# Kernel tuning notes

Measured on AMD Instinct MI355X. Metric: run time of the kernel, lower is better.

Reference implementation:

```python
import jax, jax.numpy as jnp
import numpy as np

T, D, I, E, G, LG, K = 2048, 1024, 512, 32, 8, 4, 6
SI = 2 * I  # shared expert inter dim = n_shared_experts * inter_dim
ROUTE_SCALE = 1.0


def setup_inputs() -> dict:
    key = jax.random.key(0)
    ks = jax.random.split(key, 16)
    s = 0.02
    f = jnp.float32
    return {
        "x": jax.random.normal(ks[0], (T, D), f),
        "router_w": jax.random.normal(ks[1], (E, D), f) * s,
        "router_b": jax.random.normal(ks[2], (E,), f) * s,
        "W1": jax.random.normal(ks[3], (E, D, I), f) * s,
        "b1": jax.random.normal(ks[4], (E, I), f) * s,
        "W2": jax.random.normal(ks[5], (E, D, I), f) * s,
        "b2": jax.random.normal(ks[6], (E, I), f) * s,
        "W3": jax.random.normal(ks[7], (E, I, D), f) * s,
        "b3": jax.random.normal(ks[8], (E, D), f) * s,
        "sw1": jax.random.normal(ks[9], (D, SI), f) * s,
        "sb1": jax.random.normal(ks[10], (SI,), f) * s,
        "sw2": jax.random.normal(ks[11], (D, SI), f) * s,
        "sb2": jax.random.normal(ks[12], (SI,), f) * s,
        "sw3": jax.random.normal(ks[13], (SI, D), f) * s,
        "sb3": jax.random.normal(ks[14], (D,), f) * s,
    }


def _route(x, router_w, router_b):
    # Router: softmax scores (fp32), group-limited top-k.
    logits = x @ router_w.T + router_b                      # [T, E]
    scores = jax.nn.softmax(logits.astype(jnp.float32), axis=-1)
    original = scores
    sg = scores.reshape(x.shape[0], G, E // G)              # [T, G, E/G]
    # no router bias -> group score = sum of top-2 expert scores per group
    group_scores = jnp.sum(jax.lax.top_k(sg, 2)[0], axis=-1)  # [T, G]
    _, gidx = jax.lax.top_k(group_scores, LG)               # [T, LG]
    keep = jnp.zeros((x.shape[0], G), bool).at[jnp.arange(x.shape[0])[:, None], gidx].set(True)
    masked = jnp.where(keep[:, :, None], sg, -jnp.inf).reshape(x.shape[0], E)
    _, idx = jax.lax.top_k(masked, K)                       # [T, K]
    vals = jnp.take_along_axis(original, idx, axis=1) * ROUTE_SCALE
    return vals.astype(x.dtype), idx


def reference(x, router_w, router_b, W1, b1, W2, b2, W3, b3, sw1, sb1, sw2, sb2, sw3, sb3):
    vals, idx = _route(x, router_w, router_b)
    # dense gate matrix [T, E]; top-k indices per row are distinct
    gates = jnp.zeros((x.shape[0], E), x.dtype).at[jnp.arange(x.shape[0])[:, None], idx].set(vals)
    # routed experts: Expert(x) = W3 @ silu(w1(x) * w2(x))
    h1 = jnp.einsum('td,edi->tei', x, W1) + b1              # [T, E, I]
    h2 = jnp.einsum('td,edi->tei', x, W2) + b2
    h = jax.nn.silu(h1 * h2)
    y = jnp.einsum('tei,eid->td', h * gates[:, :, None], W3) + gates @ b3
    # shared expert
    z = jax.nn.silu((x @ sw1 + sb1) * (x @ sw2 + sb2)) @ sw3 + sb3
    return y + z
```

## Files before the change

### kernel.cpp

```cpp
#include <hip/hip_runtime.h>
#include <hip/hip_bf16.h>
#include <math.h>

#define T_CONST 2048
#define D_CONST 1024
#define I_CONST 512
#define SI_CONST 1024
#define E_CONST 32
#define G_CONST 8
#define LG_CONST 4
#define KSEL 6
#define BK 32

typedef __attribute__((ext_vector_type(8))) short short8;
typedef __attribute__((ext_vector_type(4))) float floatx4;

__device__ inline unsigned pack_bf16(float a, float b) {
  __hip_bfloat162 h = __float22bfloat162_rn(float2{a, b});
  return *reinterpret_cast<unsigned*>(&h);
}

__device__ inline void gload16(const void* g, void* l) {
  __builtin_amdgcn_global_load_lds(
      (const __attribute__((address_space(1))) unsigned int*)g,
      (__attribute__((address_space(3))) unsigned int*)l, 16, 0, 0);
}

__global__ __launch_bounds__(256) void cvt_x(const float* __restrict__ in,
                                             __hip_bfloat16* __restrict__ out) {
  size_t i = ((size_t)blockIdx.x * 256 + threadIdx.x) * 4;
  float4 v = *(const float4*)&in[i];
  uint2 u{pack_bf16(v.x, v.y), pack_bf16(v.z, v.w)};
  *(uint2*)&out[i] = u;
}

__global__ __launch_bounds__(256) void cvt_rwt(const float* __restrict__ rw,
                                               float* __restrict__ rwt) {
  int i = blockIdx.x * 256 + threadIdx.x;
  int d = i >> 5, e = i & 31;
  rwt[d * 32 + e] = rw[e * D_CONST + d];
}

__global__ __launch_bounds__(256) void transpose_all(
    const float* __restrict__ W1, const float* __restrict__ W2,
    const float* __restrict__ W3, const float* __restrict__ sw1,
    const float* __restrict__ sw2, const float* __restrict__ sw3,
    __hip_bfloat16* __restrict__ W1t, __hip_bfloat16* __restrict__ W2t,
    __hip_bfloat16* __restrict__ W3t, __hip_bfloat16* __restrict__ sw1t,
    __hip_bfloat16* __restrict__ sw2t, __hip_bfloat16* __restrict__ sw3t) {
  __shared__ short tile[64 * 64];
  int b = blockIdx.x;
  const float* in;
  __hip_bfloat16* out;
  int K, N, k0, n0;
  if (b < 8192) {
    int local = b & 4095;
    int mat = local >> 7, rem = local & 127;
    K = 1024; N = 512;
    in = ((b < 4096) ? W1 : W2) + (size_t)mat * (1024 * 512);
    out = ((b < 4096) ? W1t : W2t) + (size_t)mat * (1024 * 512);
    n0 = (rem & 7) * 64; k0 = (rem >> 3) * 64;
  } else if (b < 12288) {
    int local = b - 8192;
    int mat = local >> 7, rem = local & 127;
    K = 512; N = 1024;
    in = W3 + (size_t)mat * (512 * 1024);
    out = W3t + (size_t)mat * (512 * 1024);
    n0 = (rem & 15) * 64; k0 = (rem >> 4) * 64;
  } else {
    int local = b - 12288;
    int which = local >> 8, rem = local & 255;
    K = 1024; N = 1024;
    in = which == 0 ? sw1 : which == 1 ? sw2 : sw3;
    out = which == 0 ? sw1t : which == 1 ? sw2t : sw3t;
    n0 = (rem & 15) * 64; k0 = (rem >> 4) * 64;
  }
  const int tid = threadIdx.x;
  const int u = tid & 15, tr = tid >> 4;
  float4 v[4];
#pragma unroll
  for (int r = 0; r < 4; ++r)
    v[r] = *(const float4*)&in[(size_t)(k0 + 4 * tr + r) * N + n0 + 4 * u];
#pragma unroll
  for (int j = 0; j < 4; ++j) {
    int n = 4 * u + j;
    unsigned lo = pack_bf16(((const float*)&v[0])[j], ((const float*)&v[1])[j]);
    unsigned hi = pack_bf16(((const float*)&v[2])[j], ((const float*)&v[3])[j]);
    int cu = (tr >> 1) ^ (u & 7);
    int off = n * 64 + cu * 8 + (tr & 1) * 4;
    *(uint2*)&tile[off] = uint2{lo, hi};
  }
  __syncthreads();
#pragma unroll
  for (int s2 = 0; s2 < 2; ++s2) {
    int id = tid + s2 * 256;
    int n = id >> 3, cu = id & 7;
    int cx = cu ^ ((n >> 2) & 7);
    uint4 o = *(const uint4*)&tile[n * 64 + cx * 8];
    *(uint4*)&out[(size_t)(n0 + n) * K + k0 + cu * 8] = o;
  }
}

__global__ __launch_bounds__(256) void router2(
    const float* __restrict__ x, const float* __restrict__ rwt,
    const float* __restrict__ rb, int* __restrict__ counts,
    int* __restrict__ stok, float* __restrict__ gatel) {
  const int lane = threadIdx.x & 63;
  const int wv = threadIdx.x >> 6;
  const int t = blockIdx.x * 4 + wv;
  const int e = lane & 31, h = lane >> 5;
  const float* xp = x + (size_t)t * D_CONST;
  float s = 0.f;
#pragma unroll 8
  for (int d = h; d < D_CONST; d += 2) s = fmaf(xp[d], rwt[d * 32 + e], s);
  s += __shfl_xor(s, 32);
  s += rb[e];
  float mx = s;
#pragma unroll
  for (int m = 16; m >= 1; m >>= 1) mx = fmaxf(mx, __shfl_xor(mx, m));
  float p = expf(s - mx);
  float sum = p;
#pragma unroll
  for (int m = 16; m >= 1; m >>= 1) sum += __shfl_xor(sum, m);
  float sc = p / sum;
  float a = sc, bb = __shfl_xor(a, 1);
  float hi = fmaxf(a, bb), lo = fminf(a, bb);
  float oh = __shfl_xor(hi, 2), ol = __shfl_xor(lo, 2);
  float gs = fmaxf(fmaxf(hi + oh, hi + lo), oh + ol);
  const int g = e >> 2;
  unsigned keep = 0;
  float gv = gs;
#pragma unroll
  for (int r = 0; r < LG_CONST; ++r) {
    float v = gv;
    int gi = g;
#pragma unroll
    for (int m = 16; m >= 1; m >>= 1) {
      float ov = __shfl_xor(v, m);
      int og = __shfl_xor(gi, m);
      if (ov > v || (ov == v && og < gi)) { v = ov; gi = og; }
    }
    keep |= 1u << gi;
    if (g == gi) gv = -1e30f;
  }
  float cand = ((keep >> g) & 1u) ? sc : -1e30f;
  int sel_e = -1;
  float sel_v = 0.f;
#pragma unroll
  for (int r = 0; r < KSEL; ++r) {
    float v = cand;
    int ei = e;
#pragma unroll
    for (int m = 16; m >= 1; m >>= 1) {
      float ov = __shfl_xor(v, m);
      int oe = __shfl_xor(ei, m);
      if (ov > v || (ov == v && oe < ei)) { v = ov; ei = oe; }
    }
    if (lane == r) { sel_e = ei; sel_v = v; }
    if (e == ei) cand = -1e30f;
  }
  if (lane < KSEL) {
    int pos = atomicAdd(&counts[sel_e], 1);
    stok[sel_e * T_CONST + pos] = t;
    gatel[sel_e * T_CONST + pos] = sel_v;
  }
}

__global__ __launch_bounds__(64) void plan_build(
    const int* __restrict__ counts, int* __restrict__ offsets,
    int* __restrict__ plan_up, int* __restrict__ plan_dn, int* __restrict__ meta) {
  const int lane = threadIdx.x;
  for (int i = lane; i < 128; i += 64) {
    int ent = (E_CONST << 8) | i;
    plan_up[i] = ent;
    plan_dn[i] = ent;
  }
  int cnt = (lane < E_CONST) ? counts[lane] : 0;
  int incl = cnt;
#pragma unroll
  for (int d = 1; d < 64; d <<= 1) {
    int v = __shfl_up(incl, d);
    if (lane >= d) incl += v;
  }
  if (lane < E_CONST) offsets[lane] = incl - cnt;
  if (lane == E_CONST - 1) offsets[E_CONST] = incl;
  int mbs = (cnt + 127) >> 7;
  int pm = mbs;
#pragma unroll
  for (int d = 1; d < 64; d <<= 1) {
    int v = __shfl_up(pm, d);
    if (lane >= d) pm += v;
  }
  int pmex = pm - mbs;
  if (lane < E_CONST) {
    int ub = 128 + pmex * 4, db = 128 + pmex * 8;
    for (int mb = 0; mb < mbs; ++mb) {
#pragma unroll
      for (int nb = 0; nb < 4; ++nb)
        plan_up[ub + mb * 4 + nb] = (lane << 8) | (mb << 3) | nb;
#pragma unroll
      for (int nb = 0; nb < 8; ++nb)
        plan_dn[db + mb * 8 + nb] = (lane << 8) | (mb << 3) | nb;
    }
  }
  if (lane == E_CONST - 1) {
    meta[0] = 128 + pm * 4;
    meta[1] = 128 + pm * 8;
  }
}

__global__ __launch_bounds__(256) void gather_x(
    const __hip_bfloat16* __restrict__ xbf, const int* __restrict__ counts,
    const int* __restrict__ offsets, const int* __restrict__ stok,
    const float* __restrict__ gatel, __hip_bfloat16* __restrict__ Xg,
    float* __restrict__ cgate, int* __restrict__ tcnt, int* __restrict__ tslot) {
  int e = blockIdx.x;
  int cnt = counts[e];
  int row = blockIdx.y * 16 + (threadIdx.x >> 4);
  if (row >= cnt) return;
  int seg = threadIdx.x & 15;
  int tok = stok[e * T_CONST + row];
  int dst = offsets[e] + row;
  const uint4* src = (const uint4*)(xbf + (size_t)tok * D_CONST);
  uint4* d = (uint4*)(Xg + (size_t)dst * D_CONST);
#pragma unroll
  for (int i = 0; i < 8; ++i) d[i * 16 + seg] = src[i * 16 + seg];
  if (seg == 0) {
    cgate[dst] = gatel[e * T_CONST + row];
    int sl = atomicAdd(&tcnt[tok], 1);
    tslot[tok * 8 + sl] = dst;
  }
}

__global__ __launch_bounds__(256, 2) void up_fused(
    const __hip_bfloat16* __restrict__ Xg, const __hip_bfloat16* __restrict__ xbf,
    const __hip_bfloat16* __restrict__ W1t, const __hip_bfloat16* __restrict__ W2t,
    const __hip_bfloat16* __restrict__ sw1t, const __hip_bfloat16* __restrict__ sw2t,
    const float* __restrict__ b1, const float* __restrict__ b2,
    const float* __restrict__ sb1, const float* __restrict__ sb2,
    const int* __restrict__ counts, const int* __restrict__ offsets,
    const int* __restrict__ plan, const int* __restrict__ meta,
    __hip_bfloat16* __restrict__ He, __hip_bfloat16* __restrict__ Hs) {
  const int nw = meta[0];
  const int bx = blockIdx.x;
  if (bx >= nw) return;
  const int q = nw >> 3, r = nw & 7, c = bx & 7, sl = bx >> 3;
  const int j = (c < r ? c * (q + 1) : r * (q + 1) + (c - r) * q) + sl;
  const int ent = plan[j];
  const int z = ent >> 8;
  const int m0 = ((ent >> 3) & 31) * 128;
  const int n0 = (ent & 7) * 128;
  const bool SH = (z == E_CONST);
  const int cnt = SH ? T_CONST : counts[z];
  const int base = SH ? 0 : offsets[z];

  const __hip_bfloat16* Ab = SH ? (xbf + (size_t)m0 * D_CONST)
                                : (Xg + (size_t)(base + m0) * D_CONST);
  const __hip_bfloat16* B1 = SH ? (sw1t + (size_t)n0 * D_CONST)
                                : (W1t + ((size_t)z * I_CONST + n0) * D_CONST);
  const __hip_bfloat16* B2 = SH ? (sw2t + (size_t)n0 * D_CONST)
                                : (W2t + ((size_t)z * I_CONST + n0) * D_CONST);

  __shared__ short As[3 * 4096], Bs1[3 * 4096], Bs2[3 * 4096];

  const int tid = threadIdx.x, lane = tid & 63, wv = tid >> 6;
  const int l15 = lane & 15, quad = lane >> 4;
  const int wm = wv & 1, wn = wv >> 1;
  const int lr = lane >> 2;
  const int lc = lane & 3;

  const __hip_bfloat16 *aG[2], *b1G[2], *b2G[2];
#pragma unroll
  for (int i = 0; i < 2; ++i) {
    int rr = wv * 32 + i * 16 + lr;
    int kap = lc ^ ((rr >> 1) & 3);
    aG[i]  = Ab + (size_t)rr * D_CONST + kap * 8;
    b1G[i] = B1 + (size_t)rr * D_CONST + kap * 8;
    b2G[i] = B2 + (size_t)rr * D_CONST + kap * 8;
  }
  const int ldsu = wv * 1024 + lane * 8;

  floatx4 acc1[4][4] = {};
  floatx4 acc2[4][4] = {};

  const int nIter = D_CONST / BK;

  auto stage = [&](int slot, int kk) {
    const int sb = slot * 4096;
#pragma unroll
    for (int i = 0; i < 2; ++i) {
      gload16(aG[i] + kk,  &As [sb + ldsu + i * 512]);
      gload16(b1G[i] + kk, &Bs1[sb + ldsu + i * 512]);
      gload16(b2G[i] + kk, &Bs2[sb + ldsu + i * 512]);
    }
  };

  stage(0, 0);
  stage(1, BK);
  int sl0 = 0, sl1 = 1, sl2 = 2;

  for (int s = 0; s < nIter; ++s) {
    int kn = (s + 2 < nIter) ? (s + 2) * BK : (nIter - 1) * BK;
    stage(sl2, kn);
    asm volatile("s_waitcnt vmcnt(12)" ::: "memory");
    __builtin_amdgcn_s_barrier();
    const int sb = sl0 * 4096;
    short8 a[4], x1[4], x2[4];
#pragma unroll
    for (int mi = 0; mi < 4; ++mi) {
      int m = wm * 64 + mi * 16 + l15;
      a[mi] = *(const short8*)&As[sb + m * 32 + (quad ^ ((m >> 1) & 3)) * 8];
    }
#pragma unroll
    for (int ni = 0; ni < 4; ++ni) {
      int n = wn * 64 + ni * 16 + l15;
      int uo = sb + n * 32 + (quad ^ ((n >> 1) & 3)) * 8;
      x1[ni] = *(const short8*)&Bs1[uo];
      x2[ni] = *(const short8*)&Bs2[uo];
    }
    __builtin_amdgcn_s_setprio(1);
#pragma unroll
    for (int mi = 0; mi < 4; ++mi)
#pragma unroll
      for (int ni = 0; ni < 4; ++ni) {
        acc1[mi][ni] = __builtin_amdgcn_mfma_f32_16x16x32_bf16(a[mi], x1[ni], acc1[mi][ni], 0, 0, 0);
        acc2[mi][ni] = __builtin_amdgcn_mfma_f32_16x16x32_bf16(a[mi], x2[ni], acc2[mi][ni], 0, 0, 0);
      }
    __builtin_amdgcn_s_setprio(0);
    __builtin_amdgcn_s_barrier();
    int t = sl0; sl0 = sl1; sl1 = sl2; sl2 = t;
  }
  asm volatile("s_waitcnt vmcnt(0)" ::: "memory");

  const float* pb1 = SH ? sb1 : (b1 + (size_t)z * I_CONST);
  const float* pb2 = SH ? sb2 : (b2 + (size_t)z * I_CONST);
  __hip_bfloat16* outp = SH ? (Hs + (size_t)m0 * SI_CONST + n0)
                            : (He + (size_t)(base + m0) * I_CONST + n0);
  const int ldo = SH ? SI_CONST : I_CONST;
  float c1[4], c2[4];
#pragma unroll
  for (int ni = 0; ni < 4; ++ni) {
    int n = wn * 64 + ni * 16 + l15;
    c1[ni] = pb1[n0 + n];
    c2[ni] = pb2[n0 + n];
  }
#pragma unroll
  for (int mi = 0; mi < 4; ++mi) {
#pragma unroll
    for (int reg = 0; reg < 4; ++reg) {
      int m = wm * 64 + mi * 16 + quad * 4 + reg;
      if (m0 + m >= cnt) continue;
#pragma unroll
      for (int ni = 0; ni < 4; ++ni) {
        int n = wn * 64 + ni * 16 + l15;
        float h1 = acc1[mi][ni][reg] + c1[ni];
        float h2 = acc2[mi][ni][reg] + c2[ni];
        float p = h1 * h2;
        float sg = p / (1.f + expf(-p));
        outp[(size_t)m * ldo + n] = __float2bfloat16(sg);
      }
    }
  }
}

__global__ __launch_bounds__(256, 3) void down_fused(
    const __hip_bfloat16* __restrict__ He, const __hip_bfloat16* __restrict__ Hs,
    const __hip_bfloat16* __restrict__ W3t, const __hip_bfloat16* __restrict__ sw3t,
    const float* __restrict__ b3, const float* __restrict__ sb3,
    const int* __restrict__ counts, const int* __restrict__ offsets,
    const float* __restrict__ cgate, const int* __restrict__ plan,
    const int* __restrict__ meta, float* __restrict__ Yp, float* __restrict__ out) {
  if ((int)blockIdx.x >= meta[1]) return;
  const int ent = plan[blockIdx.x];
  const int z = ent >> 8;
  const int m0 = ((ent >> 3) & 31) * 128;
  const int n0 = (ent & 7) * 128;
  const bool SH = (z == E_CONST);
  const int cnt = SH ? T_CONST : counts[z];
  const int base = SH ? 0 : offsets[z];
  const int Kd = SH ? SI_CONST : I_CONST;

  const __hip_bfloat16* Ab = SH ? (Hs + (size_t)m0 * SI_CONST)
                                : (He + (size_t)(base + m0) * I_CONST);
  const __hip_bfloat16* Bb = SH ? (sw3t + (size_t)n0 * SI_CONST)
                                : (W3t + ((size_t)z * D_CONST + n0) * I_CONST);

  __shared__ short As[3 * 4096], Bs[3 * 4096];

  const int tid = threadIdx.x, lane = tid & 63, wv = tid >> 6;
  const int l15 = lane & 15, quad = lane >> 4;
  const int wm = wv & 1, wn = wv >> 1;
  const int lr = lane >> 2, lc = lane & 3;

  const __hip_bfloat16 *aG[2], *bG[2];
#pragma unroll
  for (int i = 0; i < 2; ++i) {
    int rr = wv * 32 + i * 16 + lr;
    int kap = lc ^ ((rr >> 1) & 3);
    aG[i] = Ab + (size_t)rr * Kd + kap * 8;
    bG[i] = Bb + (size_t)rr * Kd + kap * 8;
  }
  const int ldsu = wv * 1024 + lane * 8;

  floatx4 acc[4][4] = {};
  const int nIter = Kd / BK;

  auto stage = [&](int slot, int kk) {
    const int sb = slot * 4096;
#pragma unroll
    for (int i = 0; i < 2; ++i) {
      gload16(aG[i] + kk, &As[sb + ldsu + i * 512]);
      gload16(bG[i] + kk, &Bs[sb + ldsu + i * 512]);
    }
  };

  stage(0, 0);
  stage(1, BK);
  int sl0 = 0, sl1 = 1, sl2 = 2;

  for (int s = 0; s < nIter; ++s) {
    int kn = (s + 2 < nIter) ? (s + 2) * BK : (nIter - 1) * BK;
    stage(sl2, kn);
    asm volatile("s_waitcnt vmcnt(8)" ::: "memory");
    __builtin_amdgcn_s_barrier();
    const int sb = sl0 * 4096;
    short8 a[4], bbf[4];
#pragma unroll
    for (int mi = 0; mi < 4; ++mi) {
      int m = wm * 64 + mi * 16 + l15;
      a[mi] = *(const short8*)&As[sb + m * 32 + (quad ^ ((m >> 1) & 3)) * 8];
    }
#pragma unroll
    for (int ni = 0; ni < 4; ++ni) {
      int n = wn * 64 + ni * 16 + l15;
      bbf[ni] = *(const short8*)&Bs[sb + n * 32 + (quad ^ ((n >> 1) & 3)) * 8];
    }
    __builtin_amdgcn_s_setprio(1);
#pragma unroll
    for (int mi = 0; mi < 4; ++mi)
#pragma unroll
      for (int ni = 0; ni < 4; ++ni)
        acc[mi][ni] = __builtin_amdgcn_mfma_f32_16x16x32_bf16(a[mi], bbf[ni], acc[mi][ni], 0, 0, 0);
    __builtin_amdgcn_s_setprio(0);
    __builtin_amdgcn_s_barrier();
    int t = sl0; sl0 = sl1; sl1 = sl2; sl2 = t;
  }
  asm volatile("s_waitcnt vmcnt(0)" ::: "memory");

  float bias[4];
#pragma unroll
  for (int ni = 0; ni < 4; ++ni) {
    int n = n0 + wn * 64 + ni * 16 + l15;
    bias[ni] = SH ? sb3[n] : b3[(size_t)z * D_CONST + n];
  }
#pragma unroll
  for (int mi = 0; mi < 4; ++mi) {
#pragma unroll
    for (int reg = 0; reg < 4; ++reg) {
      int m = wm * 64 + mi * 16 + quad * 4 + reg;
      if (m0 + m >= cnt) continue;
#pragma unroll
      for (int ni = 0; ni < 4; ++ni) {
        int n = n0 + wn * 64 + ni * 16 + l15;
        float v = acc[mi][ni][reg] + bias[ni];
        if (SH) {
          out[(size_t)(m0 + m) * D_CONST + n] = v;
        } else {
          int grow = base + m0 + m;
          Yp[(size_t)grow * D_CONST + n] = cgate[grow] * v;
        }
      }
    }
  }
}

__global__ __launch_bounds__(256) void combine(
    const float* __restrict__ Yp, const int* __restrict__ tslot,
    float* __restrict__ out) {
  const int t = blockIdx.x;
  const int d = threadIdx.x * 4;
  const int* ts = &tslot[t * 8];
  float4 o = *(const float4*)&out[(size_t)t * D_CONST + d];
#pragma unroll
  for (int k = 0; k < KSEL; ++k) {
    float4 y = *(const float4*)&Yp[(size_t)ts[k] * D_CONST + d];
    o.x += y.x; o.y += y.y; o.z += y.z; o.w += y.w;
  }
  *(float4*)&out[(size_t)t * D_CONST + d] = o;
}

extern "C" void kernel_launch(void* const* d_in, const int* in_sizes, int n_in,
                              void* d_out, int out_size, void* d_ws, size_t ws_size,
                              hipStream_t stream) {
  const float* x   = (const float*)d_in[0];
  const float* rw  = (const float*)d_in[1];
  const float* rb  = (const float*)d_in[2];
  const float* W1  = (const float*)d_in[3];
  const float* b1  = (const float*)d_in[4];
  const float* W2  = (const float*)d_in[5];
  const float* b2  = (const float*)d_in[6];
  const float* W3  = (const float*)d_in[7];
  const float* b3  = (const float*)d_in[8];
  const float* sw1 = (const float*)d_in[9];
  const float* sb1 = (const float*)d_in[10];
  const float* sw2 = (const float*)d_in[11];
  const float* sb2 = (const float*)d_in[12];
  const float* sw3 = (const float*)d_in[13];
  const float* sb3 = (const float*)d_in[14];
  float* out = (float*)d_out;

  char* w = (char*)d_ws;
  size_t off = 0;
  auto alloc = [&](size_t bytes) {
    char* p = w + off;
    off += (bytes + 255) & ~(size_t)255;
    return p;
  };
  int* counts = (int*)alloc(E_CONST * 4);
  int* offsets = (int*)alloc((E_CONST + 1) * 4);
  int* meta = (int*)alloc(16);
  int* plan_up = (int*)alloc(768 * 4);
  int* plan_dn = (int*)alloc(1280 * 4);
  int* tcnt = (int*)alloc((size_t)T_CONST * 4);
  int* tslot = (int*)alloc((size_t)T_CONST * 8 * 4);
  int* stok = (int*)alloc((size_t)E_CONST * T_CONST * 4);
  float* gatel = (float*)alloc((size_t)E_CONST * T_CONST * 4);
  float* rwt = (float*)alloc((size_t)D_CONST * E_CONST * 4);
  float* cgate = (float*)alloc((size_t)T_CONST * KSEL * 4);
  __hip_bfloat16* x_bf = (__hip_bfloat16*)alloc((size_t)T_CONST * D_CONST * 2);
  __hip_bfloat16* Xg = (__hip_bfloat16*)alloc((size_t)(T_CONST * KSEL + 128) * D_CONST * 2);
  __hip_bfloat16* W1t = (__hip_bfloat16*)alloc((size_t)E_CONST * D_CONST * I_CONST * 2);
  __hip_bfloat16* W2t = (__hip_bfloat16*)alloc((size_t)E_CONST * D_CONST * I_CONST * 2);
  __hip_bfloat16* W3t = (__hip_bfloat16*)alloc((size_t)E_CONST * I_CONST * D_CONST * 2);
  __hip_bfloat16* sw1t = (__hip_bfloat16*)alloc((size_t)D_CONST * SI_CONST * 2);
  __hip_bfloat16* sw2t = (__hip_bfloat16*)alloc((size_t)D_CONST * SI_CONST * 2);
  __hip_bfloat16* sw3t = (__hip_bfloat16*)alloc((size_t)SI_CONST * D_CONST * 2);
  __hip_bfloat16* He = (__hip_bfloat16*)alloc((size_t)(T_CONST * KSEL + 128) * I_CONST * 2);
  __hip_bfloat16* Hs = (__hip_bfloat16*)alloc((size_t)T_CONST * SI_CONST * 2);
  float* Yp = (float*)W1t;

  hipMemsetAsync(counts, 0, E_CONST * sizeof(int), stream);
  hipMemsetAsync(tcnt, 0, (size_t)T_CONST * sizeof(int), stream);
  cvt_rwt<<<(D_CONST * E_CONST) / 256, 256, 0, stream>>>(rw, rwt);
  cvt_x<<<(T_CONST * D_CONST) / 1024, 256, 0, stream>>>(x, x_bf);
  transpose_all<<<13056, 256, 0, stream>>>(W1, W2, W3, sw1, sw2, sw3,
                                           W1t, W2t, W3t, sw1t, sw2t, sw3t);
  router2<<<T_CONST / 4, 256, 0, stream>>>(x, rwt, rb, counts, stok, gatel);
  plan_build<<<1, 64, 0, stream>>>(counts, offsets, plan_up, plan_dn, meta);
  gather_x<<<dim3(E_CONST, T_CONST / 16), 256, 0, stream>>>(
      x_bf, counts, offsets, stok, gatel, Xg, cgate, tcnt, tslot);
  up_fused<<<768, 256, 0, stream>>>(
      Xg, x_bf, W1t, W2t, sw1t, sw2t, b1, b2, sb1, sb2, counts, offsets,
      plan_up, meta, He, Hs);
  down_fused<<<1280, 256, 0, stream>>>(
      He, Hs, W3t, sw3t, b3, sb3, counts, offsets, cgate, plan_dn, meta, Yp, out);
  combine<<<T_CONST, 256, 0, stream>>>(Yp, tslot, out);
}
```

Baseline: 473.6 us.

## Fuse prep kernels, widen transpose tiles, and double-buffer down GEMM

Merges the x conversion, router-weight transpose and weight transpose/bf16 conversion into one prep kernel, cutting two launches. Each transpose block now handles a 256x64 tile instead of 64x64, so 512-byte contiguous output rows replace 128-byte ones, with a new XOR swizzle on a larger shared tile. The down GEMM also moves from a 3-stage to a 2-stage LDS pipeline, which lowers shared memory use and may raise occupancy but leaves less prefetch distance to hide load latency.

```diff
diff --git a/kernel.cpp b/kernel.cpp
--- a/kernel.cpp
+++ b/kernel.cpp
@@ -26,78 +26,90 @@
       (__attribute__((address_space(3))) unsigned int*)l, 16, 0, 0);
 }
 
-__global__ __launch_bounds__(256) void cvt_x(const float* __restrict__ in,
-                                             __hip_bfloat16* __restrict__ out) {
-  size_t i = ((size_t)blockIdx.x * 256 + threadIdx.x) * 4;
-  float4 v = *(const float4*)&in[i];
-  uint2 u{pack_bf16(v.x, v.y), pack_bf16(v.z, v.w)};
-  *(uint2*)&out[i] = u;
-}
-
-__global__ __launch_bounds__(256) void cvt_rwt(const float* __restrict__ rw,
-                                               float* __restrict__ rwt) {
-  int i = blockIdx.x * 256 + threadIdx.x;
-  int d = i >> 5, e = i & 31;
-  rwt[d * 32 + e] = rw[e * D_CONST + d];
-}
-
-__global__ __launch_bounds__(256) void transpose_all(
+__global__ __launch_bounds__(256) void prep_all(
+    const float* __restrict__ x, const float* __restrict__ rw,
     const float* __restrict__ W1, const float* __restrict__ W2,
     const float* __restrict__ W3, const float* __restrict__ sw1,
     const float* __restrict__ sw2, const float* __restrict__ sw3,
+    __hip_bfloat16* __restrict__ x_bf, float* __restrict__ rwt,
     __hip_bfloat16* __restrict__ W1t, __hip_bfloat16* __restrict__ W2t,
     __hip_bfloat16* __restrict__ W3t, __hip_bfloat16* __restrict__ sw1t,
     __hip_bfloat16* __restrict__ sw2t, __hip_bfloat16* __restrict__ sw3t) {
-  __shared__ short tile[64 * 64];
-  int b = blockIdx.x;
+  const int b = blockIdx.x;
+  const int tid = threadIdx.x;
+  if (b >= 3264) {
+    int lb = b - 3264;
+    if (lb < 512) {
+      size_t base = (size_t)lb * 4096 + tid * 4;
+#pragma unroll
+      for (int it = 0; it < 4; ++it) {
+        float4 v = *(const float4*)&x[base + it * 1024];
+        uint2 u{pack_bf16(v.x, v.y), pack_bf16(v.z, v.w)};
+        *(uint2*)&x_bf[base + it * 1024] = u;
+      }
+    } else {
+      int lb2 = lb - 512;
+#pragma unroll
+      for (int it = 0; it < 4; ++it) {
+        int i = lb2 * 1024 + it * 256 + tid;
+        int d = i >> 5, e = i & 31;
+        rwt[d * 32 + e] = rw[e * D_CONST + d];
+      }
+    }
+    return;
+  }
   const float* in;
   __hip_bfloat16* out;
   int K, N, k0, n0;
-  if (b < 8192) {
-    int local = b & 4095;
-    int mat = local >> 7, rem = local & 127;
+  if (b < 2048) {
+    int mat = b >> 5, rem = b & 31;
     K = 1024; N = 512;
-    in = ((b < 4096) ? W1 : W2) + (size_t)mat * (1024 * 512);
-    out = ((b < 4096) ? W1t : W2t) + (size_t)mat * (1024 * 512);
-    n0 = (rem & 7) * 64; k0 = (rem >> 3) * 64;
-  } else if (b < 12288) {
-    int local = b - 8192;
-    int mat = local >> 7, rem = local & 127;
+    int e = mat & 31;
+    in = ((mat < 32) ? W1 : W2) + (size_t)e * (1024 * 512);
+    out = ((mat < 32) ? W1t : W2t) + (size_t)e * (1024 * 512);
+    k0 = (rem >> 3) * 256; n0 = (rem & 7) * 64;
+  } else if (b < 3072) {
+    int local = b - 2048;
+    int e = local >> 5, rem = local & 31;
     K = 512; N = 1024;
-    in = W3 + (size_t)mat * (512 * 1024);
-    out = W3t + (size_t)mat * (512 * 1024);
-    n0 = (rem & 15) * 64; k0 = (rem >> 4) * 64;
+    in = W3 + (size_t)e * (512 * 1024);
+    out = W3t + (size_t)e * (512 * 1024);
+    k0 = (rem >> 4) * 256; n0 = (rem & 15) * 64;
   } else {
-    int local = b - 12288;
-    int which = local >> 8, rem = local & 255;
+    int local = b - 3072;
+    int which = local >> 6, rem = local & 63;
     K = 1024; N = 1024;
     in = which == 0 ? sw1 : which == 1 ? sw2 : sw3;
     out = which == 0 ? sw1t : which == 1 ? sw2t : sw3t;
-    n0 = (rem & 15) * 64; k0 = (rem >> 4) * 64;
-  }
-  const int tid = threadIdx.x;
+    k0 = (rem >> 4) * 256; n0 = (rem & 15) * 64;
+  }
+  __shared__ short tile[64 * 256];
   const int u = tid & 15, tr = tid >> 4;
-  float4 v[4];
-#pragma unroll
-  for (int r = 0; r < 4; ++r)
-    v[r] = *(const float4*)&in[(size_t)(k0 + 4 * tr + r) * N + n0 + 4 * u];
-#pragma unroll
-  for (int j = 0; j < 4; ++j) {
-    int n = 4 * u + j;
-    unsigned lo = pack_bf16(((const float*)&v[0])[j], ((const float*)&v[1])[j]);
-    unsigned hi = pack_bf16(((const float*)&v[2])[j], ((const float*)&v[3])[j]);
-    int cu = (tr >> 1) ^ (u & 7);
-    int off = n * 64 + cu * 8 + (tr & 1) * 4;
-    *(uint2*)&tile[off] = uint2{lo, hi};
+#pragma unroll
+  for (int sub = 0; sub < 4; ++sub) {
+    float4 v[4];
+#pragma unroll
+    for (int r = 0; r < 4; ++r)
+      v[r] = *(const float4*)&in[(size_t)(k0 + sub * 64 + 4 * tr + r) * N + n0 + 4 * u];
+    int kb = sub * 64 + 4 * tr;
+    int chunk = kb >> 3, half = (kb >> 2) & 1;
+#pragma unroll
+    for (int j = 0; j < 4; ++j) {
+      int n = 4 * u + j;
+      unsigned lo = pack_bf16(((const float*)&v[0])[j], ((const float*)&v[1])[j]);
+      unsigned hi = pack_bf16(((const float*)&v[2])[j], ((const float*)&v[3])[j]);
+      int cx = chunk ^ ((n >> 2) & 7) ^ ((n & 3) << 3);
+      *(uint2*)&tile[n * 256 + cx * 8 + half * 4] = uint2{lo, hi};
+    }
   }
   __syncthreads();
-#pragma unroll
-  for (int s2 = 0; s2 < 2; ++s2) {
-    int id = tid + s2 * 256;
-    int n = id >> 3, cu = id & 7;
-    int cx = cu ^ ((n >> 2) & 7);
-    uint4 o = *(const uint4*)&tile[n * 64 + cx * 8];
-    *(uint4*)&out[(size_t)(n0 + n) * K + k0 + cu * 8] = o;
+  const int n_ = tid >> 5, c_ = tid & 31;
+#pragma unroll
+  for (int p = 0; p < 8; ++p) {
+    int n = p * 8 + n_;
+    int cx = c_ ^ ((n >> 2) & 7) ^ ((n & 3) << 3);
+    uint4 o = *(const uint4*)&tile[n * 256 + cx * 8];
+    *(uint4*)&out[(size_t)(n0 + n) * K + k0 + c_ * 8] = o;
   }
 }
 
@@ -385,7 +397,7 @@
   const __hip_bfloat16* Bb = SH ? (sw3t + (size_t)n0 * SI_CONST)
                                 : (W3t + ((size_t)z * D_CONST + n0) * I_CONST);
 
-  __shared__ short As[3 * 4096], Bs[3 * 4096];
+  __shared__ short As[2 * 4096], Bs[2 * 4096];
 
   const int tid = threadIdx.x, lane = tid & 63, wv = tid >> 6;
   const int l15 = lane & 15, quad = lane >> 4;
@@ -415,15 +427,14 @@
   };
 
   stage(0, 0);
-  stage(1, BK);
-  int sl0 = 0, sl1 = 1, sl2 = 2;
+  int cur = 0;
 
   for (int s = 0; s < nIter; ++s) {
-    int kn = (s + 2 < nIter) ? (s + 2) * BK : (nIter - 1) * BK;
-    stage(sl2, kn);
-    asm volatile("s_waitcnt vmcnt(8)" ::: "memory");
+    int kn = (s + 1 < nIter) ? (s + 1) * BK : s * BK;
+    stage(cur ^ 1, kn);
+    asm volatile("s_waitcnt vmcnt(4)" ::: "memory");
     __builtin_amdgcn_s_barrier();
-    const int sb = sl0 * 4096;
+    const int sb = cur * 4096;
     short8 a[4], bbf[4];
 #pragma unroll
     for (int mi = 0; mi < 4; ++mi) {
@@ -443,7 +454,7 @@
         acc[mi][ni] = __builtin_amdgcn_mfma_f32_16x16x32_bf16(a[mi], bbf[ni], acc[mi][ni], 0, 0, 0);
     __builtin_amdgcn_s_setprio(0);
     __builtin_amdgcn_s_barrier();
-    int t = sl0; sl0 = sl1; sl1 = sl2; sl2 = t;
+    cur ^= 1;
   }
   asm volatile("s_waitcnt vmcnt(0)" ::: "memory");
 
@@ -541,10 +552,8 @@
 
   hipMemsetAsync(counts, 0, E_CONST * sizeof(int), stream);
   hipMemsetAsync(tcnt, 0, (size_t)T_CONST * sizeof(int), stream);
-  cvt_rwt<<<(D_CONST * E_CONST) / 256, 256, 0, stream>>>(rw, rwt);
-  cvt_x<<<(T_CONST * D_CONST) / 1024, 256, 0, stream>>>(x, x_bf);
-  transpose_all<<<13056, 256, 0, stream>>>(W1, W2, W3, sw1, sw2, sw3,
-                                           W1t, W2t, W3t, sw1t, sw2t, sw3t);
+  prep_all<<<3808, 256, 0, stream>>>(x, rw, W1, W2, W3, sw1, sw2, sw3,
+                                     x_bf, rwt, W1t, W2t, W3t, sw1t, sw2t, sw3t);
   router2<<<T_CONST / 4, 256, 0, stream>>>(x, rwt, rb, counts, stok, gatel);
   plan_build<<<1, 64, 0, stream>>>(counts, offsets, plan_up, plan_dn, meta);
   gather_x<<<dim3(E_CONST, T_CONST / 16), 256, 0, stream>>>(
```

Result: faster. 459.4 us (-3.0%).
